# Performance work log

Measured on AMD Instinct MI355X. Metric: run time of the kernel, lower is better.

## Reference

```python
import jax, jax.numpy as jnp
import numpy as np


def _wasserstein_1d(xs, a, b, p):
    # POT-style 1D OT loss on shared sorted support xs: sum over merged
    # quantile levels of |F_a^{-1}(q) - F_b^{-1}(q)|^p * dq  (no p-th root).
    n = xs.shape[0]
    cdf_a = jnp.cumsum(a)
    cdf_b = jnp.cumsum(b)
    qs = jnp.sort(jnp.concatenate([cdf_a, cdf_b]))  # [2n] merged quantile levels
    qa = xs[jnp.clip(jnp.searchsorted(cdf_a, qs), 0, n - 1)]
    qb = xs[jnp.clip(jnp.searchsorted(cdf_b, qs), 0, n - 1)]
    qs_pad = jnp.concatenate([jnp.zeros((1,), qs.dtype), qs])
    delta = qs_pad[1:] - qs_pad[:-1]
    return jnp.sum(delta * jnp.abs(qa - qb) ** p)


def setup_inputs() -> dict:
    key = jax.random.key(0)
    k1, k2 = jax.random.split(key)
    N = 8388608      # samples
    NBINS = 10       # discretization
    G = 4            # number of groups
    acts = jax.random.normal(k1, (N,), dtype=jnp.float32)
    group_labels = jax.random.randint(k2, (N,), 0, G, dtype=jnp.int32)
    bary_est = jnp.ones((NBINS,), jnp.float32) / NBINS  # learned barycenter param, init 1/n
    return {"acts": acts, "bary_est": bary_est, "group_labels": group_labels,
            "nbins": NBINS, "n_groups": G}


def reference(acts, bary_est, group_labels, nbins, n_groups):
    r = 1.0 / nbins
    locs = jnp.arange(0, 1, r, dtype=acts.dtype)              # [nbins] bin centers
    c = jax.nn.sigmoid(acts) - 0.0001                         # [N] cdf-mapped samples
    # triangular-kernel soft histogram contributions: [N, nbins]
    K = jax.nn.relu(r - jnp.abs(c[:, None] - locs[None, :]))
    # per-group bin counts (torch.unique returns sorted labels 0..G-1)
    counts = jax.ops.segment_sum(K, group_labels, num_segments=n_groups)  # [G, nbins]
    h = counts + 0.0001
    h = h / jnp.sum(h, axis=1, keepdims=True)   # HistoBin norm
    h = h / jnp.sum(h, axis=1, keepdims=True)   # genHists renorm (mathematical no-op, kept for fidelity)
    xs = jnp.arange(nbins, dtype=acts.dtype)    # POT support bins 0..n-1
    losses = jax.vmap(lambda hg: _wasserstein_1d(xs, hg, bary_est, 2))(h)  # [G]
    loss = jnp.sum(losses).reshape(1)
    return loss, bary_est
```

## Files before the change

kernel.cpp:

```cpp
#include <hip/hip_runtime.h>

#define NBINS 10
#define NG 4
#define NH (NG * NBINS)
#define TPB 128
#define NROWS NH

__device__ __forceinline__ void proc4(float4 a, int4 g, float* col) {
    const float xv[4] = {a.x, a.y, a.z, a.w};
    const int   gv[4] = {g.x, g.y, g.z, g.w};
    #pragma unroll
    for (int e = 0; e < 4; ++e) {
        float ex = __expf(-xv[e]);
        float c = __builtin_amdgcn_rcpf(1.0f + ex) - 0.0001f;
        float fj = floorf(c * 10.0f);
        int j0 = (int)fj;
        int b = gv[e] * NBINS;
        float t = c - 0.1f * fj;
        float w0 = 0.1f - t;
        float w1 = t;
        if (j0 < 0) w0 = 0.0f;
        if (j0 > NBINS - 2) w1 = 0.0f;
        int r0 = b + max(j0, 0);
        int r1 = b + min(j0 + 1, NBINS - 1);
        col[r0 * TPB] += w0;
        col[r1 * TPB] += w1;
    }
}

__global__ void __launch_bounds__(TPB) wb_hist(const float4* __restrict__ acts,
                                               const int4* __restrict__ labels,
                                               const float* __restrict__ acts_s,
                                               const int* __restrict__ labels_s,
                                               float* __restrict__ parts,
                                               int n4, int n, int nparts) {
    __shared__ float lh[NROWS * TPB];
    const int tid = threadIdx.x;
    for (int i = tid; i < NROWS * TPB; i += TPB) lh[i] = 0.0f;
    __syncthreads();

    float* col = &lh[tid];
    const int gsz = gridDim.x * TPB;
    int idx = blockIdx.x * TPB + tid;
    for (; idx + 3 * gsz < n4; idx += 4 * gsz) {
        float4 a0 = acts[idx];
        float4 a1 = acts[idx + gsz];
        float4 a2 = acts[idx + 2 * gsz];
        float4 a3 = acts[idx + 3 * gsz];
        int4 g0 = labels[idx];
        int4 g1 = labels[idx + gsz];
        int4 g2 = labels[idx + 2 * gsz];
        int4 g3 = labels[idx + 3 * gsz];
        proc4(a0, g0, col); proc4(a1, g1, col);
        proc4(a2, g2, col); proc4(a3, g3, col);
    }
    for (; idx < n4; idx += gsz) proc4(acts[idx], labels[idx], col);

    if (blockIdx.x == 0 && tid == 0) {
        for (int i = n4 * 4; i < n; ++i) {
            float ex = __expf(-acts_s[i]);
            float c = __builtin_amdgcn_rcpf(1.0f + ex) - 0.0001f;
            float fj = floorf(c * 10.0f);
            int j0 = (int)fj;
            int b = labels_s[i] * NBINS;
            float t = c - 0.1f * fj;
            float w0 = 0.1f - t, w1 = t;
            if (j0 < 0) w0 = 0.0f;
            if (j0 > NBINS - 2) w1 = 0.0f;
            col[(b + max(j0, 0)) * TPB] += w0;
            col[(b + min(j0 + 1, NBINS - 1)) * TPB] += w1;
        }
    }
    __syncthreads();

    if (tid < NH) {
        float s = 0.0f;
        for (int k = 0; k < TPB; ++k)
            s += lh[tid * TPB + ((tid + k) & (TPB - 1))];
        parts[tid * nparts + blockIdx.x] = s;
    }
}

__global__ void __launch_bounds__(1024) wb_final(const float4* __restrict__ parts4,
                                                 const float* __restrict__ bary,
                                                 float* __restrict__ out, int nparts) {
    __shared__ float hist[NH];
    __shared__ float bsh[NBINS];
    __shared__ float losses[NG];

    if (threadIdx.x < NBINS) {
        float b = bary[threadIdx.x];
        bsh[threadIdx.x] = b;
        out[1 + threadIdx.x] = b;
    }

    const int q4 = nparts >> 2;
    int wave = threadIdx.x >> 6, lane = threadIdx.x & 63;
    for (int j = wave; j < NH; j += 16) {
        float s = 0.0f;
        for (int i = lane; i < q4; i += 64) {
            float4 v = parts4[j * q4 + i];
            s += (v.x + v.y) + (v.z + v.w);
        }
        #pragma unroll
        for (int off = 32; off; off >>= 1) s += __shfl_down(s, off);
        if (lane == 0) hist[j] = s;
    }
    __syncthreads();

    if (threadIdx.x < NG) {
        const int gI = threadIdx.x;
        float h[NBINS];
        float s = 0.0f;
        #pragma unroll
        for (int j = 0; j < NBINS; ++j) { h[j] = hist[gI * NBINS + j] + 0.0001f; s += h[j]; }
        #pragma unroll
        for (int j = 0; j < NBINS; ++j) h[j] /= s;
        float s2 = 0.0f;
        #pragma unroll
        for (int j = 0; j < NBINS; ++j) s2 += h[j];
        #pragma unroll
        for (int j = 0; j < NBINS; ++j) h[j] /= s2;

        float cdfa[NBINS], cdfb[NBINS];
        float acc = 0.0f;
        #pragma unroll
        for (int j = 0; j < NBINS; ++j) { acc += h[j]; cdfa[j] = acc; }
        acc = 0.0f;
        #pragma unroll
        for (int j = 0; j < NBINS; ++j) { acc += bsh[j]; cdfb[j] = acc; }
        float T = fmaxf(cdfa[NBINS - 1], cdfb[NBINS - 1]);
        cdfa[NBINS - 1] = T;
        cdfb[NBINS - 1] = T;

        float loss = 0.0f, lo_a = 0.0f;
        #pragma unroll
        for (int i = 0; i < NBINS; ++i) {
            float hi_a = cdfa[i];
            float lo_b = 0.0f;
            #pragma unroll
            for (int j = 0; j < NBINS; ++j) {
                float hi_b = cdfb[j];
                float ov = fminf(hi_a, hi_b) - fmaxf(lo_a, lo_b);
                float w = (float)((i - j) * (i - j));
                loss += fmaxf(ov, 0.0f) * w;
                lo_b = hi_b;
            }
            lo_a = hi_a;
        }
        losses[gI] = loss;
    }
    __syncthreads();
    if (threadIdx.x == 0)
        out[0] = losses[0] + losses[1] + losses[2] + losses[3];
}

extern "C" void kernel_launch(void* const* d_in, const int* in_sizes, int n_in,
                              void* d_out, int out_size, void* d_ws, size_t ws_size,
                              hipStream_t stream) {
    const float* acts   = (const float*)d_in[0];
    const float* bary   = (const float*)d_in[1];
    const int*   labels = (const int*)d_in[2];
    float* outp  = (float*)d_out;
    float* parts = (float*)d_ws;
    int N  = in_sizes[0];
    int n4 = N >> 2;

    int nparts = 2048;
    while (nparts > 4 && (size_t)NH * nparts * sizeof(float) > ws_size) nparts >>= 1;

    wb_hist<<<nparts, TPB, 0, stream>>>((const float4*)acts, (const int4*)labels,
                                        acts, labels, parts, n4, N, nparts);
    wb_final<<<1, 1024, 0, stream>>>((const float4*)parts, bary, outp, nparts);
}
```

Measured before the change: 33.03 us.

## Fuse histogram and loss into one kernel with atomic last-block finalize

Merges the histogram and final-reduction kernels into one launch. Per-block partial histograms are atomically added into a small array of 64 group slots, and a ticket counter picks the last block to finish, which reduces the slots and computes the Wasserstein loss. The main loop is also unrolled from 4 to 8 loads per iteration to keep more memory requests in flight. This adds a memset launch and atomic contention on the slot array in place of the second kernel launch.

```diff
diff --git a/kernel.cpp b/kernel.cpp
--- a/kernel.cpp
+++ b/kernel.cpp
@@ -4,7 +4,9 @@
 #define NG 4
 #define NH (NG * NBINS)
 #define TPB 128
-#define NROWS NH
+#define NBLOCKS 2048
+#define GSHIFT 5
+#define NGROUPS (NBLOCKS >> GSHIFT)
 
 __device__ __forceinline__ void proc4(float4 a, int4 g, float* col) {
     const float xv[4] = {a.x, a.y, a.z, a.w};
@@ -28,31 +30,48 @@
     }
 }
 
-__global__ void __launch_bounds__(TPB) wb_hist(const float4* __restrict__ acts,
-                                               const int4* __restrict__ labels,
-                                               const float* __restrict__ acts_s,
-                                               const int* __restrict__ labels_s,
-                                               float* __restrict__ parts,
-                                               int n4, int n, int nparts) {
-    __shared__ float lh[NROWS * TPB];
+__global__ void __launch_bounds__(TPB) wb_fused(const float4* __restrict__ acts,
+                                                const int4* __restrict__ labels,
+                                                const float* __restrict__ acts_s,
+                                                const int* __restrict__ labels_s,
+                                                const float* __restrict__ bary,
+                                                float* __restrict__ out,
+                                                float* __restrict__ parts2,
+                                                unsigned int* __restrict__ ticket,
+                                                int n4, int n, int nblocks) {
+    __shared__ float lh[NH * TPB];
+    float* hist   = &lh[0];
+    float* losses = &lh[48];
+    volatile unsigned int* lastflag = (volatile unsigned int*)&lh[56];
+
     const int tid = threadIdx.x;
-    for (int i = tid; i < NROWS * TPB; i += TPB) lh[i] = 0.0f;
+    for (int i = tid; i < NH * TPB; i += TPB) lh[i] = 0.0f;
     __syncthreads();
 
     float* col = &lh[tid];
     const int gsz = gridDim.x * TPB;
     int idx = blockIdx.x * TPB + tid;
-    for (; idx + 3 * gsz < n4; idx += 4 * gsz) {
+    for (; idx + 7 * gsz < n4; idx += 8 * gsz) {
         float4 a0 = acts[idx];
         float4 a1 = acts[idx + gsz];
         float4 a2 = acts[idx + 2 * gsz];
         float4 a3 = acts[idx + 3 * gsz];
+        float4 a4 = acts[idx + 4 * gsz];
+        float4 a5 = acts[idx + 5 * gsz];
+        float4 a6 = acts[idx + 6 * gsz];
+        float4 a7 = acts[idx + 7 * gsz];
         int4 g0 = labels[idx];
         int4 g1 = labels[idx + gsz];
         int4 g2 = labels[idx + 2 * gsz];
         int4 g3 = labels[idx + 3 * gsz];
+        int4 g4 = labels[idx + 4 * gsz];
+        int4 g5 = labels[idx + 5 * gsz];
+        int4 g6 = labels[idx + 6 * gsz];
+        int4 g7 = labels[idx + 7 * gsz];
         proc4(a0, g0, col); proc4(a1, g1, col);
         proc4(a2, g2, col); proc4(a3, g3, col);
+        proc4(a4, g4, col); proc4(a5, g5, col);
+        proc4(a6, g6, col); proc4(a7, g7, col);
     }
     for (; idx < n4; idx += gsz) proc4(acts[idx], labels[idx], col);
 
@@ -77,39 +96,33 @@
         float s = 0.0f;
         for (int k = 0; k < TPB; ++k)
             s += lh[tid * TPB + ((tid + k) & (TPB - 1))];
-        parts[tid * nparts + blockIdx.x] = s;
-    }
-}
-
-__global__ void __launch_bounds__(1024) wb_final(const float4* __restrict__ parts4,
-                                                 const float* __restrict__ bary,
-                                                 float* __restrict__ out, int nparts) {
-    __shared__ float hist[NH];
-    __shared__ float bsh[NBINS];
-    __shared__ float losses[NG];
-
-    if (threadIdx.x < NBINS) {
-        float b = bary[threadIdx.x];
-        bsh[threadIdx.x] = b;
-        out[1 + threadIdx.x] = b;
-    }
-
-    const int q4 = nparts >> 2;
-    int wave = threadIdx.x >> 6, lane = threadIdx.x & 63;
-    for (int j = wave; j < NH; j += 16) {
-        float s = 0.0f;
-        for (int i = lane; i < q4; i += 64) {
-            float4 v = parts4[j * q4 + i];
-            s += (v.x + v.y) + (v.z + v.w);
-        }
-        #pragma unroll
-        for (int off = 32; off; off >>= 1) s += __shfl_down(s, off);
-        if (lane == 0) hist[j] = s;
+        atomicAdd(&parts2[tid * NGROUPS + (blockIdx.x >> GSHIFT)], s);
     }
     __syncthreads();
 
-    if (threadIdx.x < NG) {
-        const int gI = threadIdx.x;
+    if (tid == 0) {
+        __threadfence();
+        unsigned int old = atomicAdd(ticket, 1u);
+        *lastflag = (old == (unsigned int)nblocks - 1u) ? 1u : 0u;
+    }
+    __syncthreads();
+    if (*lastflag == 0u) return;
+
+    __threadfence();
+    if (tid < NH) {
+        float s = 0.0f;
+        #pragma unroll 8
+        for (int g = 0; g < NGROUPS; ++g)
+            s += __hip_atomic_load(&parts2[tid * NGROUPS + g],
+                                   __ATOMIC_RELAXED, __HIP_MEMORY_SCOPE_AGENT);
+        hist[tid] = s;
+    }
+    if (tid >= NH && tid < NH + NBINS)
+        out[1 + (tid - NH)] = bary[tid - NH];
+    __syncthreads();
+
+    if (tid < NG) {
+        const int gI = tid;
         float h[NBINS];
         float s = 0.0f;
         #pragma unroll
@@ -128,7 +141,7 @@
         for (int j = 0; j < NBINS; ++j) { acc += h[j]; cdfa[j] = acc; }
         acc = 0.0f;
         #pragma unroll
-        for (int j = 0; j < NBINS; ++j) { acc += bsh[j]; cdfb[j] = acc; }
+        for (int j = 0; j < NBINS; ++j) { acc += bary[j]; cdfb[j] = acc; }
         float T = fmaxf(cdfa[NBINS - 1], cdfb[NBINS - 1]);
         cdfa[NBINS - 1] = T;
         cdfb[NBINS - 1] = T;
@@ -151,7 +164,7 @@
         losses[gI] = loss;
     }
     __syncthreads();
-    if (threadIdx.x == 0)
+    if (tid == 0)
         out[0] = losses[0] + losses[1] + losses[2] + losses[3];
 }
 
@@ -161,15 +174,14 @@
     const float* acts   = (const float*)d_in[0];
     const float* bary   = (const float*)d_in[1];
     const int*   labels = (const int*)d_in[2];
-    float* outp  = (float*)d_out;
-    float* parts = (float*)d_ws;
+    float* outp   = (float*)d_out;
+    float* parts2 = (float*)d_ws;
+    unsigned int* ticket = (unsigned int*)((char*)d_ws + NH * NGROUPS * sizeof(float));
     int N  = in_sizes[0];
     int n4 = N >> 2;
 
-    int nparts = 2048;
-    while (nparts > 4 && (size_t)NH * nparts * sizeof(float) > ws_size) nparts >>= 1;
-
-    wb_hist<<<nparts, TPB, 0, stream>>>((const float4*)acts, (const int4*)labels,
-                                        acts, labels, parts, n4, N, nparts);
-    wb_final<<<1, 1024, 0, stream>>>((const float4*)parts, bary, outp, nparts);
+    hipMemsetAsync(d_ws, 0, (NH * NGROUPS + 1) * sizeof(float), stream);
+    wb_fused<<<NBLOCKS, TPB, 0, stream>>>((const float4*)acts, (const int4*)labels,
+                                          acts, labels, bary, outp,
+                                          parts2, ticket, n4, N, NBLOCKS);
 }
```

After: 80.13 us. 143% more time.

## Pack count and offset into one LDS update per sample

Applied to the files above, without the earlier changes.

Each sample now does a single shared-memory add of PACK+t into its lower bin instead of two weighted adds. At reduction time the packed value is split into a count (floor of acc/PACK) and a residual sum of t. Each bin's mass is then rebuilt as 0.1*count - sum_t plus the previous bin's sum_t, taken via a lane shuffle. The block size also drops to 64 threads across 4096 fixed blocks, with the inner loop unrolled by 8. This halves the LDS read-modify-write traffic, but float precision limits how many samples one accumulator can hold before the packed residual loses accuracy. The workspace-size check is also removed, so it assumes ws holds 40*4096 floats.

```diff
diff --git a/kernel.cpp b/kernel.cpp
--- a/kernel.cpp
+++ b/kernel.cpp
@@ -3,8 +3,9 @@
 #define NBINS 10
 #define NG 4
 #define NH (NG * NBINS)
-#define TPB 128
-#define NROWS NH
+#define TPB 64
+#define NBLOCKS 4096
+#define PACK 32.0f
 
 __device__ __forceinline__ void proc4(float4 a, int4 g, float* col) {
     const float xv[4] = {a.x, a.y, a.z, a.w};
@@ -15,44 +16,48 @@
         float c = __builtin_amdgcn_rcpf(1.0f + ex) - 0.0001f;
         float fj = floorf(c * 10.0f);
         int j0 = (int)fj;
-        int b = gv[e] * NBINS;
         float t = c - 0.1f * fj;
-        float w0 = 0.1f - t;
-        float w1 = t;
-        if (j0 < 0) w0 = 0.0f;
-        if (j0 > NBINS - 2) w1 = 0.0f;
-        int r0 = b + max(j0, 0);
-        int r1 = b + min(j0 + 1, NBINS - 1);
-        col[r0 * TPB] += w0;
-        col[r1 * TPB] += w1;
+        int row = gv[e] * NBINS + max(j0, 0);
+        col[row * TPB] += PACK + t;
     }
 }
 
-__global__ void __launch_bounds__(TPB) wb_hist(const float4* __restrict__ acts,
-                                               const int4* __restrict__ labels,
-                                               const float* __restrict__ acts_s,
-                                               const int* __restrict__ labels_s,
-                                               float* __restrict__ parts,
-                                               int n4, int n, int nparts) {
-    __shared__ float lh[NROWS * TPB];
+__global__ void __launch_bounds__(TPB, 4) wb_hist(const float4* __restrict__ acts,
+                                                  const int4* __restrict__ labels,
+                                                  const float* __restrict__ acts_s,
+                                                  const int* __restrict__ labels_s,
+                                                  float* __restrict__ parts,
+                                                  int n4, int n, int nparts) {
+    __shared__ float lh[NH * TPB];
     const int tid = threadIdx.x;
-    for (int i = tid; i < NROWS * TPB; i += TPB) lh[i] = 0.0f;
+    #pragma unroll
+    for (int i = 0; i < NH; ++i) lh[i * TPB + tid] = 0.0f;
     __syncthreads();
 
     float* col = &lh[tid];
     const int gsz = gridDim.x * TPB;
     int idx = blockIdx.x * TPB + tid;
-    for (; idx + 3 * gsz < n4; idx += 4 * gsz) {
+    for (; idx + 7 * gsz < n4; idx += 8 * gsz) {
         float4 a0 = acts[idx];
         float4 a1 = acts[idx + gsz];
         float4 a2 = acts[idx + 2 * gsz];
         float4 a3 = acts[idx + 3 * gsz];
+        float4 a4 = acts[idx + 4 * gsz];
+        float4 a5 = acts[idx + 5 * gsz];
+        float4 a6 = acts[idx + 6 * gsz];
+        float4 a7 = acts[idx + 7 * gsz];
         int4 g0 = labels[idx];
         int4 g1 = labels[idx + gsz];
         int4 g2 = labels[idx + 2 * gsz];
         int4 g3 = labels[idx + 3 * gsz];
+        int4 g4 = labels[idx + 4 * gsz];
+        int4 g5 = labels[idx + 5 * gsz];
+        int4 g6 = labels[idx + 6 * gsz];
+        int4 g7 = labels[idx + 7 * gsz];
         proc4(a0, g0, col); proc4(a1, g1, col);
         proc4(a2, g2, col); proc4(a3, g3, col);
+        proc4(a4, g4, col); proc4(a5, g5, col);
+        proc4(a6, g6, col); proc4(a7, g7, col);
     }
     for (; idx < n4; idx += gsz) proc4(acts[idx], labels[idx], col);
 
@@ -62,22 +67,24 @@
             float c = __builtin_amdgcn_rcpf(1.0f + ex) - 0.0001f;
             float fj = floorf(c * 10.0f);
             int j0 = (int)fj;
-            int b = labels_s[i] * NBINS;
             float t = c - 0.1f * fj;
-            float w0 = 0.1f - t, w1 = t;
-            if (j0 < 0) w0 = 0.0f;
-            if (j0 > NBINS - 2) w1 = 0.0f;
-            col[(b + max(j0, 0)) * TPB] += w0;
-            col[(b + min(j0 + 1, NBINS - 1)) * TPB] += w1;
+            col[(labels_s[i] * NBINS + max(j0, 0)) * TPB] += PACK + t;
         }
     }
     __syncthreads();
 
     if (tid < NH) {
-        float s = 0.0f;
-        for (int k = 0; k < TPB; ++k)
-            s += lh[tid * TPB + ((tid + k) & (TPB - 1))];
-        parts[tid * nparts + blockIdx.x] = s;
+        float n_sum = 0.0f, s_sum = 0.0f;
+        for (int k = 0; k < TPB; ++k) {
+            float acc = lh[tid * TPB + ((tid + k) & (TPB - 1))];
+            float nc = floorf(acc * (1.0f / PACK));
+            n_sum += nc;
+            s_sum += acc - PACK * nc;
+        }
+        float s_prev = __shfl_up(s_sum, 1);
+        if ((tid % NBINS) == 0) s_prev = 0.0f;
+        float hb = 0.1f * n_sum - s_sum + s_prev;
+        parts[tid * nparts + blockIdx.x] = hb;
     }
 }
 
@@ -166,10 +173,7 @@
     int N  = in_sizes[0];
     int n4 = N >> 2;
 
-    int nparts = 2048;
-    while (nparts > 4 && (size_t)NH * nparts * sizeof(float) > ws_size) nparts >>= 1;
-
-    wb_hist<<<nparts, TPB, 0, stream>>>((const float4*)acts, (const int4*)labels,
-                                        acts, labels, parts, n4, N, nparts);
-    wb_final<<<1, 1024, 0, stream>>>((const float4*)parts, bary, outp, nparts);
+    wb_hist<<<NBLOCKS, TPB, 0, stream>>>((const float4*)acts, (const int4*)labels,
+                                         acts, labels, parts, n4, N, NBLOCKS);
+    wb_final<<<1, 1024, 0, stream>>>((const float4*)parts, bary, outp, NBLOCKS);
 }
```

New measurement: 40.03 us. 1.21x slower.
